# Kernel optimization log

Measured on AMD Instinct MI355X. Metric: run time of the kernel, lower is better.

The kernel has to match this reference:

```python
import jax, jax.numpy as jnp
import numpy as np

B, T, I, H, K = 32, 1024, 512, 512, 2


def _causal_conv1d(x_bit, w_hik, b_h):
    # x_bit: [B, I, T]; left-pad K-1 zeros (ConstantPad1d((K-1, 0)))
    xp = jnp.pad(x_bit, ((0, 0), (0, 0), (K - 1, 0)))
    y = jax.lax.conv_general_dilated(
        xp, w_hik, window_strides=(1,), padding='VALID',
        dimension_numbers=('NCH', 'OIH', 'NCH'))  # [B, H, T]
    return y + b_h[None, :, None]


def setup_inputs() -> dict:
    key = jax.random.key(0)
    k1, k2, k3 = jax.random.split(key, 3)
    bound = 1.0 / np.sqrt(I * K)  # torch Conv1d default init scale
    return {
        'inputs': jax.random.normal(k1, (B, T, I), dtype=jnp.float32),
        'init_state': jnp.zeros((B, H), dtype=jnp.float32),
        'Wz': jax.random.uniform(k2, (H, I, K), jnp.float32, -bound, bound),
        'bz': jnp.zeros((H,), dtype=jnp.float32),
        'Wf': jax.random.uniform(k3, (H, I, K), jnp.float32, -bound, bound),
        'bf': jnp.zeros((H,), dtype=jnp.float32),
    }


def reference(inputs, init_state, Wz, bz, Wf, bf):
    # init_state is accepted but unused in the original forward (mode='f').
    x = inputs.transpose(0, 2, 1)                      # [B, I, T]
    raw_f = _causal_conv1d(x, Wf, bf).transpose(0, 2, 1)  # [B, T, H]
    raw_z = _causal_conv1d(x, Wz, bz).transpose(0, 2, 1)  # [B, T, H]

    log_f = jax.nn.log_sigmoid(raw_f)
    log_one_minus_f = jax.nn.log_sigmoid(-raw_f)
    log_z = jax.nn.log_sigmoid(raw_z)

    # recurrent_gates[t] = sum_{s>t} log_f[s]  (suffix sum of log_f over time, excluding t=0 shift)
    rg = log_f[:, 1:, :]                               # [B, T-1, H]
    cs = jnp.cumsum(rg, axis=1)
    rg = rg - cs + cs[:, -1:, :]
    rg = jnp.concatenate([rg, jnp.zeros((inputs.shape[0], 1, rg.shape[2]), dtype=rg.dtype)], axis=1)  # [B, T, H]

    log_hidden = jax.lax.cumlogsumexp(log_z + log_one_minus_f + rg, axis=1)
    hidden = jnp.exp(log_hidden - rg)
    return hidden
```

## Files before the change

### kernel.cpp

```cpp
#include <hip/hip_runtime.h>
#include <hip/hip_bf16.h>
#include <cstddef>
#include <cstdint>

#define B_  32
#define T_  1024
#define I_  512
#define H_  512
#define M_  (B_ * T_)
#define TP_ 1025

typedef __bf16 bf16x8  __attribute__((ext_vector_type(8)));
typedef float  floatx4 __attribute__((ext_vector_type(4)));
typedef unsigned short ushort8v __attribute__((ext_vector_type(8)));
typedef unsigned long long u64;

__device__ __forceinline__ unsigned short f2bf(float f) {
    return __builtin_bit_cast(unsigned short, (__bf16)f);
}
__device__ __forceinline__ float sigm(float x) {
    return __builtin_amdgcn_rcpf(1.f + __expf(-x));
}

#define GLL(src, dst) __builtin_amdgcn_global_load_lds( \
    (const __attribute__((address_space(1))) void*)(src), \
    (__attribute__((address_space(3))) void*)(dst), 16, 0, 0)

#define NB_BUILD 8200
#define NB_PACK  512
#define NB_ZERO  256

__global__ __launch_bounds__(256) void prep(const float* __restrict__ x,
                                            const float* __restrict__ Wf,
                                            const float* __restrict__ Wz,
                                            unsigned short* __restrict__ Ab2,
                                            unsigned short* __restrict__ Wq,
                                            uint4* __restrict__ HpubZ,
                                            uint32_t* __restrict__ tickets) {
    if (blockIdx.x < NB_BUILD) {
        int g = blockIdx.x * 256 + threadIdx.x;
        int idx8 = g << 3;
        int row = idx8 >> 9;
        int col = idx8 & 511;
        int b    = (int)((unsigned)row / TP_);
        int trow = row - b * TP_;
        ushort8v o = {0, 0, 0, 0, 0, 0, 0, 0};
        if (trow > 0) {
            const float* src = &x[((size_t)b * T_ + (trow - 1)) * I_ + col];
            float4 v0 = *(const float4*)src;
            float4 v1 = *(const float4*)(src + 4);
            o[0] = f2bf(v0.x); o[1] = f2bf(v0.y); o[2] = f2bf(v0.z); o[3] = f2bf(v0.w);
            o[4] = f2bf(v1.x); o[5] = f2bf(v1.y); o[6] = f2bf(v1.z); o[7] = f2bf(v1.w);
        }
        *(ushort8v*)&Ab2[(size_t)idx8] = o;
    } else if (blockIdx.x < NB_BUILD + NB_PACK) {
        int cid = (blockIdx.x - NB_BUILD) * 256 + threadIdx.x;
        int lane = cid & 63;
        int c    = (cid >> 6) & 3;
        int wn   = (cid >> 8) & 1;
        int ksub = (cid >> 9) & 31;
        int ni   = (cid >> 14) & 3;
        int gate = (cid >> 16) & 1;
        int n_col = ni * 128 + wn * 64 + c * 16 + (lane & 15);
        const float* G = gate ? Wz : Wf;
        ushort8v o;
        #pragma unroll
        for (int j = 0; j < 8; ++j) {
            int k   = ksub * 32 + (lane >> 4) * 8 + j;
            int tap = k >> 9;
            int i   = k & 511;
            o[j] = f2bf(G[n_col * (I_ * 2) + i * 2 + tap]);
        }
        *(ushort8v*)&Wq[(size_t)cid * 8] = o;
    } else {
        int g = (blockIdx.x - NB_BUILD - NB_PACK) * 256 + threadIdx.x;
        HpubZ[g] = make_uint4(0, 0, 0, 0);
        if (g < 128) tickets[g] = 0;
    }
}

__global__ __launch_bounds__(256, 2) void mfma_gemm_scan(
        const unsigned short* __restrict__ Ab2,
        const unsigned short* __restrict__ Wq,
        const float* __restrict__ biasF,
        const float* __restrict__ biasZ,
        float* __restrict__ out,
        u64* __restrict__ Hpub,
        uint32_t* __restrict__ tickets) {
    __shared__ unsigned short smem[24576];
    __shared__ uint32_t pos_s;

    const int tid = threadIdx.x;
    const int bid = blockIdx.x;
    const int x   = bid & 7;
    const int ni  = (bid >> 3) & 3;
    const int q   = bid >> 5;
    const int b   = ((q & 3) << 3) | x;
    const int chain = ni * 32 + b;
    if (tid == 0) pos_s = atomicAdd(&tickets[chain], 1u);
    __syncthreads();
    const int pos = (int)pos_s;
    const int h0  = ni * 128;
    const int browBase = b * TP_ + pos * 128;

    const int lane = tid & 63;
    const int wave = tid >> 6;
    const int wm   = wave >> 1, wn = wave & 1;
    const int lm   = lane & 15, quad = lane >> 4;

    const int c0 = wave * 128 + lane;
    const int c1 = c0 + 64;
    const int r0 = c0 >> 2, q0 = (c0 & 3) ^ ((r0 >> 2) & 3);
    const int r1 = c1 >> 2, q1 = (c1 & 3) ^ ((r1 >> 2) & 3);

    const unsigned short* pA0 = Ab2 + (size_t)(browBase + r0) * 512 + q0 * 8;
    const unsigned short* pA1 = Ab2 + (size_t)(browBase + r1) * 512 + q1 * 8;

    const unsigned short* pBF = Wq + ni * 131072 + wn * 2048 + lane * 8;

    int offA[4];
    #pragma unroll
    for (int r = 0; r < 4; ++r) {
        int ml = wm * 64 + r * 16 + lm;
        offA[r] = (4 * ml + (quad ^ ((ml >> 2) & 3))) * 8;
    }

    floatx4 accF[4][4] = {};
    floatx4 accZ[4][4] = {};
    bf16x8 bfA[4], bzA[4], bfB[4], bzB[4];

#define ISSUE_A(ksub, sA) do {                                          \
        const int aoff_ = (((ksub) >> 4) * 512) + (((ksub) & 15) * 32); \
        GLL(pA0 + aoff_, (sA) + wave * 1024);                           \
        GLL(pA1 + aoff_, (sA) + wave * 1024 + 512);                     \
    } while (0)

#define LOADB(ksub, BF, BZ) do {                                        \
        const unsigned short* pf_ = pBF + (ksub) * 4096;                \
        _Pragma("unroll")                                               \
        for (int c = 0; c < 4; ++c) {                                   \
            BF[c] = *(const bf16x8*)(pf_ + c * 512);                    \
            BZ[c] = *(const bf16x8*)(pf_ + 524288 + c * 512);           \
        }                                                               \
    } while (0)

#define MFMA32(AF, BF, BZ) do {                                         \
        __builtin_amdgcn_s_setprio(1);                                  \
        _Pragma("unroll")                                               \
        for (int r = 0; r < 4; ++r) {                                   \
            _Pragma("unroll")                                           \
            for (int c = 0; c < 4; ++c) {                               \
                accF[r][c] = __builtin_amdgcn_mfma_f32_16x16x32_bf16(   \
                                AF[r], BF[c], accF[r][c], 0, 0, 0);     \
                accZ[r][c] = __builtin_amdgcn_mfma_f32_16x16x32_bf16(   \
                                AF[r], BZ[c], accZ[r][c], 0, 0, 0);     \
            }                                                           \
        }                                                               \
        __builtin_amdgcn_s_setprio(0);                                  \
    } while (0)

#define RDA(slot, AF) do {                                              \
        _Pragma("unroll")                                               \
        for (int r = 0; r < 4; ++r)                                     \
            AF[r] = *(const bf16x8*)((slot) + offA[r]);                 \
    } while (0)

#define ROT() do { unsigned short* t_ = s0; s0 = s1; s1 = s2; s2 = t_; } while (0)

    unsigned short* s0 = smem;
    unsigned short* s1 = smem + 4096;
    unsigned short* s2 = smem + 8192;

    ISSUE_A(0, s0);
    ISSUE_A(1, s1);
    LOADB(0, bfA, bzA);

    {
        asm volatile("s_waitcnt vmcnt(0)");
        __builtin_amdgcn_s_barrier();
        asm volatile("" ::: "memory");
        bf16x8 af_[4];
        RDA(s0, af_);
        LOADB(1, bfB, bzB);
        ISSUE_A(2, s2);
        __builtin_amdgcn_sched_barrier(0);
        MFMA32(af_, bfA, bzA);
        ROT();
    }
    for (int p = 0; p < 14; ++p) {
        const int k1 = 2 * p + 1;
        {
            asm volatile("s_waitcnt vmcnt(2)");
            __builtin_amdgcn_s_barrier();
            asm volatile("" ::: "memory");
            bf16x8 af_[4];
            RDA(s0, af_);
            LOADB(k1 + 1, bfA, bzA);
            ISSUE_A(k1 + 2, s2);
            __builtin_amdgcn_sched_barrier(0);
            MFMA32(af_, bfB, bzB);
            ROT();
        }
        {
            asm volatile("s_waitcnt vmcnt(2)");
            __builtin_amdgcn_s_barrier();
            asm volatile("" ::: "memory");
            bf16x8 af_[4];
            RDA(s0, af_);
            LOADB(k1 + 2, bfB, bzB);
            ISSUE_A(k1 + 3, s2);
            __builtin_amdgcn_sched_barrier(0);
            MFMA32(af_, bfA, bzA);
            ROT();
        }
    }
    {
        asm volatile("s_waitcnt vmcnt(2)");
        __builtin_amdgcn_s_barrier();
        asm volatile("" ::: "memory");
        bf16x8 af_[4];
        RDA(s0, af_);
        LOADB(30, bfA, bzA);
        ISSUE_A(31, s2);
        __builtin_amdgcn_sched_barrier(0);
        MFMA32(af_, bfB, bzB);
        ROT();
    }
    {
        asm volatile("s_waitcnt vmcnt(2)");
        __builtin_amdgcn_s_barrier();
        asm volatile("" ::: "memory");
        bf16x8 af_[4];
        RDA(s0, af_);
        LOADB(31, bfB, bzB);
        __builtin_amdgcn_sched_barrier(0);
        MFMA32(af_, bfA, bzA);
        ROT();
    }
    {
        asm volatile("s_waitcnt vmcnt(0)");
        __builtin_amdgcn_s_barrier();
        asm volatile("" ::: "memory");
        bf16x8 af_[4];
        RDA(s0, af_);
        __builtin_amdgcn_sched_barrier(0);
        MFMA32(af_, bfB, bzB);
    }
#undef ISSUE_A
#undef LOADB
#undef MFMA32
#undef RDA
#undef ROT
    __syncthreads();

    float bfv[4], bzv[4];
    #pragma unroll
    for (int c = 0; c < 4; ++c) {
        int hc = h0 + wn * 64 + c * 16 + lm;
        bfv[c] = biasF[hc];
        bzv[c] = biasZ[hc];
    }

    float2* seg  = (float2*)smem;
    float*  hinL = (float*)&smem[16384];

    #pragma unroll
    for (int r = 0; r < 4; ++r) {
        const int sid = wm * 16 + r * 4 + quad;
        #pragma unroll
        for (int c = 0; c < 4; ++c) {
            float A = 1.f, C = 0.f;
            #pragma unroll
            for (int v = 0; v < 4; ++v) {
                float f = sigm(accF[r][c][v] + bfv[c]);
                float z = sigm(accZ[r][c][v] + bzv[c]);
                accF[r][c][v] = f;
                accZ[r][c][v] = z;
                A *= f;
                C = fmaf(f, C - z, z);
            }
            seg[sid * 128 + wn * 64 + c * 16 + lm] = make_float2(A, C);
        }
    }
    __syncthreads();

    if (tid < 128) {
        float At = 1.f, Ct = 0.f;
        #pragma unroll 8
        for (int s = 0; s < 32; ++s) {
            float2 sc = seg[s * 128 + tid];
            Ct = fmaf(sc.x, Ct, sc.y);
            At *= sc.x;
        }
        float Hin = 0.f;
        if (pos > 0) {
            u64* p = &Hpub[((size_t)(pos - 1) * 128 + chain) * 128 + tid];
            u64 v;
            while (((v = atomicAdd(p, 0ull)) >> 32) == 0ull)
                __builtin_amdgcn_s_sleep(2);
            Hin = __uint_as_float((uint32_t)v);
        }
        if (pos < 7) {
            float Hout = fmaf(At, Hin, Ct);
            u64 pv = 0x100000000ull | (u64)__float_as_uint(Hout);
            atomicExch(&Hpub[((size_t)pos * 128 + chain) * 128 + tid], pv);
        }
        float run = Hin;
        #pragma unroll 8
        for (int s = 0; s < 32; ++s) {
            hinL[s * 128 + tid] = run;
            float2 sc = seg[s * 128 + tid];
            run = fmaf(sc.x, run, sc.y);
        }
    }
    __syncthreads();

    const int rowBase = b * T_ + pos * 128;
    #pragma unroll
    for (int r = 0; r < 4; ++r) {
        const int sid = wm * 16 + r * 4 + quad;
        #pragma unroll
        for (int c = 0; c < 4; ++c) {
            const int hc = h0 + wn * 64 + c * 16 + lm;
            float hs = hinL[sid * 128 + (hc - h0)];
            #pragma unroll
            for (int v = 0; v < 4; ++v) {
                float f = accF[r][c][v];
                float z = accZ[r][c][v];
                hs = fmaf(f, hs - z, z);
                const size_t row = (size_t)(rowBase + wm * 64 + r * 16 + quad * 4 + v);
                out[row * H_ + hc] = hs;
            }
        }
    }
}

extern "C" void kernel_launch(void* const* d_in, const int* in_sizes, int n_in,
                              void* d_out, int out_size, void* d_ws, size_t ws_size,
                              hipStream_t stream) {
    const float* x  = (const float*)d_in[0];
    const float* Wz = (const float*)d_in[2];
    const float* bz = (const float*)d_in[3];
    const float* Wf = (const float*)d_in[4];
    const float* bf = (const float*)d_in[5];
    float* out = (float*)d_out;

    char* ws = (char*)d_ws;
    unsigned short* Ab2  = (unsigned short*)(ws);
    unsigned short* Wq   = (unsigned short*)(ws + (size_t)34 * 1024 * 1024);
    u64*            Hpub = (u64*)(ws + (size_t)36 * 1024 * 1024);
    uint32_t*       tkt  = (uint32_t*)(ws + (size_t)37 * 1024 * 1024);

    prep<<<NB_BUILD + NB_PACK + NB_ZERO, 256, 0, stream>>>(
        x, Wf, Wz, Ab2, Wq, (uint4*)Hpub, tkt);

    mfma_gemm_scan<<<1024, 256, 0, stream>>>(Ab2, Wq, bf, bz, out, Hpub, tkt);
}
```

Before: 191.8 us.

## Fuse fp32-to-bf16 input conversion and causal shift into GEMM A-tile loads

```diff
diff --git a/kernel.cpp b/kernel.cpp
--- a/kernel.cpp
+++ b/kernel.cpp
@@ -8,7 +8,6 @@
 #define I_  512
 #define H_  512
 #define M_  (B_ * T_)
-#define TP_ 1025
 
 typedef __bf16 bf16x8  __attribute__((ext_vector_type(8)));
 typedef float  floatx4 __attribute__((ext_vector_type(4)));
@@ -22,39 +21,16 @@
     return __builtin_amdgcn_rcpf(1.f + __expf(-x));
 }
 
-#define GLL(src, dst) __builtin_amdgcn_global_load_lds( \
-    (const __attribute__((address_space(1))) void*)(src), \
-    (__attribute__((address_space(3))) void*)(dst), 16, 0, 0)
-
-#define NB_BUILD 8200
 #define NB_PACK  512
 #define NB_ZERO  256
 
-__global__ __launch_bounds__(256) void prep(const float* __restrict__ x,
-                                            const float* __restrict__ Wf,
+__global__ __launch_bounds__(256) void prep(const float* __restrict__ Wf,
                                             const float* __restrict__ Wz,
-                                            unsigned short* __restrict__ Ab2,
                                             unsigned short* __restrict__ Wq,
                                             uint4* __restrict__ HpubZ,
                                             uint32_t* __restrict__ tickets) {
-    if (blockIdx.x < NB_BUILD) {
-        int g = blockIdx.x * 256 + threadIdx.x;
-        int idx8 = g << 3;
-        int row = idx8 >> 9;
-        int col = idx8 & 511;
-        int b    = (int)((unsigned)row / TP_);
-        int trow = row - b * TP_;
-        ushort8v o = {0, 0, 0, 0, 0, 0, 0, 0};
-        if (trow > 0) {
-            const float* src = &x[((size_t)b * T_ + (trow - 1)) * I_ + col];
-            float4 v0 = *(const float4*)src;
-            float4 v1 = *(const float4*)(src + 4);
-            o[0] = f2bf(v0.x); o[1] = f2bf(v0.y); o[2] = f2bf(v0.z); o[3] = f2bf(v0.w);
-            o[4] = f2bf(v1.x); o[5] = f2bf(v1.y); o[6] = f2bf(v1.z); o[7] = f2bf(v1.w);
-        }
-        *(ushort8v*)&Ab2[(size_t)idx8] = o;
-    } else if (blockIdx.x < NB_BUILD + NB_PACK) {
-        int cid = (blockIdx.x - NB_BUILD) * 256 + threadIdx.x;
+    if (blockIdx.x < NB_PACK) {
+        int cid = blockIdx.x * 256 + threadIdx.x;
         int lane = cid & 63;
         int c    = (cid >> 6) & 3;
         int wn   = (cid >> 8) & 1;
@@ -73,14 +49,14 @@
         }
         *(ushort8v*)&Wq[(size_t)cid * 8] = o;
     } else {
-        int g = (blockIdx.x - NB_BUILD - NB_PACK) * 256 + threadIdx.x;
+        int g = (blockIdx.x - NB_PACK) * 256 + threadIdx.x;
         HpubZ[g] = make_uint4(0, 0, 0, 0);
         if (g < 128) tickets[g] = 0;
     }
 }
 
 __global__ __launch_bounds__(256, 2) void mfma_gemm_scan(
-        const unsigned short* __restrict__ Ab2,
+        const float* __restrict__ x,
         const unsigned short* __restrict__ Wq,
         const float* __restrict__ biasF,
         const float* __restrict__ biasZ,
@@ -92,16 +68,16 @@
 
     const int tid = threadIdx.x;
     const int bid = blockIdx.x;
-    const int x   = bid & 7;
+    const int xcd = bid & 7;
     const int ni  = (bid >> 3) & 3;
     const int q   = bid >> 5;
-    const int b   = ((q & 3) << 3) | x;
+    const int b   = ((q & 3) << 3) | xcd;
     const int chain = ni * 32 + b;
     if (tid == 0) pos_s = atomicAdd(&tickets[chain], 1u);
     __syncthreads();
     const int pos = (int)pos_s;
     const int h0  = ni * 128;
-    const int browBase = b * TP_ + pos * 128;
+    const int trow0 = pos * 128;
 
     const int lane = tid & 63;
     const int wave = tid >> 6;
@@ -113,8 +89,13 @@
     const int r0 = c0 >> 2, q0 = (c0 & 3) ^ ((r0 >> 2) & 3);
     const int r1 = c1 >> 2, q1 = (c1 & 3) ^ ((r1 >> 2) & 3);
 
-    const unsigned short* pA0 = Ab2 + (size_t)(browBase + r0) * 512 + q0 * 8;
-    const unsigned short* pA1 = Ab2 + (size_t)(browBase + r1) * 512 + q1 * 8;
+    const float* zp = (const float*)(Hpub + (size_t)7 * 128 * 128);
+    const float* pt0_r0 = (pos == 0 && r0 == 0)
+        ? (zp + q0 * 8)
+        : (x + (size_t)(b * T_ + trow0 + r0 - 1) * 512 + q0 * 8);
+    const float* pt1_r0 = x + (size_t)(b * T_ + trow0 + r0) * 512 + q0 * 8;
+    const float* pt0_r1 = x + (size_t)(b * T_ + trow0 + r1 - 1) * 512 + q1 * 8;
+    const float* pt1_r1 = x + (size_t)(b * T_ + trow0 + r1) * 512 + q1 * 8;
 
     const unsigned short* pBF = Wq + ni * 131072 + wn * 2048 + lane * 8;
 
@@ -128,11 +109,29 @@
     floatx4 accF[4][4] = {};
     floatx4 accZ[4][4] = {};
     bf16x8 bfA[4], bzA[4], bfB[4], bzB[4];
-
-#define ISSUE_A(ksub, sA) do {                                          \
-        const int aoff_ = (((ksub) >> 4) * 512) + (((ksub) & 15) * 32); \
-        GLL(pA0 + aoff_, (sA) + wave * 1024);                           \
-        GLL(pA1 + aoff_, (sA) + wave * 1024 + 512);                     \
+    float4 av0, av1, av2, av3;
+
+#define LOADA(ksub) do {                                                \
+        const float* b0_ = ((ksub) & 16) ? pt1_r0 : pt0_r0;             \
+        const float* b1_ = ((ksub) & 16) ? pt1_r1 : pt0_r1;             \
+        const int io_ = ((ksub) & 15) * 32;                             \
+        av0 = *(const float4*)(b0_ + io_);                              \
+        av1 = *(const float4*)(b0_ + io_ + 4);                          \
+        av2 = *(const float4*)(b1_ + io_);                              \
+        av3 = *(const float4*)(b1_ + io_ + 4);                          \
+    } while (0)
+
+#define CVTW(slot) do {                                                 \
+        bf16x8 w0_, w1_;                                                \
+        _Pragma("unroll")                                               \
+        for (int j = 0; j < 4; ++j) {                                   \
+            w0_[j]     = (__bf16)av0[j];                                \
+            w0_[4 + j] = (__bf16)av1[j];                                \
+            w1_[j]     = (__bf16)av2[j];                                \
+            w1_[4 + j] = (__bf16)av3[j];                                \
+        }                                                               \
+        *(bf16x8*)((slot) + c0 * 8) = w0_;                              \
+        *(bf16x8*)((slot) + c1 * 8) = w1_;                              \
     } while (0)
 
 #define LOADB(ksub, BF, BZ) do {                                        \
@@ -165,92 +164,86 @@
             AF[r] = *(const bf16x8*)((slot) + offA[r]);                 \
     } while (0)
 
-#define ROT() do { unsigned short* t_ = s0; s0 = s1; s1 = s2; s2 = t_; } while (0)
-
-    unsigned short* s0 = smem;
-    unsigned short* s1 = smem + 4096;
-    unsigned short* s2 = smem + 8192;
-
-    ISSUE_A(0, s0);
-    ISSUE_A(1, s1);
+#define WAITBAR() do {                                                  \
+        asm volatile("s_waitcnt vmcnt(0) lgkmcnt(0)");                  \
+        __builtin_amdgcn_s_barrier();                                   \
+        asm volatile("" ::: "memory");                                  \
+    } while (0)
+
+    unsigned short* sl0 = smem;
+    unsigned short* sl1 = smem + 4096;
+
+    LOADA(0);
+    asm volatile("s_waitcnt vmcnt(0)");
+    CVTW(sl0);
+    LOADA(1);
     LOADB(0, bfA, bzA);
 
+    for (int p = 0; p < 14; ++p) {
+        const int k = 2 * p;
+        {
+            WAITBAR();
+            LOADB(k + 1, bfB, bzB);
+            CVTW(sl1);
+            LOADA(k + 2);
+            __builtin_amdgcn_sched_barrier(0);
+            bf16x8 af_[4];
+            RDA(sl0, af_);
+            MFMA32(af_, bfA, bzA);
+        }
+        {
+            WAITBAR();
+            LOADB(k + 2, bfA, bzA);
+            CVTW(sl0);
+            LOADA(k + 3);
+            __builtin_amdgcn_sched_barrier(0);
+            bf16x8 af_[4];
+            RDA(sl1, af_);
+            MFMA32(af_, bfB, bzB);
+        }
+    }
     {
-        asm volatile("s_waitcnt vmcnt(0)");
-        __builtin_amdgcn_s_barrier();
-        asm volatile("" ::: "memory");
+        WAITBAR();
+        LOADB(29, bfB, bzB);
+        CVTW(sl1);
+        LOADA(30);
+        __builtin_amdgcn_sched_barrier(0);
         bf16x8 af_[4];
-        RDA(s0, af_);
-        LOADB(1, bfB, bzB);
-        ISSUE_A(2, s2);
+        RDA(sl0, af_);
+        MFMA32(af_, bfA, bzA);
+    }
+    {
+        WAITBAR();
+        LOADB(30, bfA, bzA);
+        CVTW(sl0);
+        LOADA(31);
         __builtin_amdgcn_sched_barrier(0);
+        bf16x8 af_[4];
+        RDA(sl1, af_);
+        MFMA32(af_, bfB, bzB);
+    }
+    {
+        WAITBAR();
+        LOADB(31, bfB, bzB);
+        CVTW(sl1);
+        __builtin_amdgcn_sched_barrier(0);
+        bf16x8 af_[4];
+        RDA(sl0, af_);
         MFMA32(af_, bfA, bzA);
-        ROT();
-    }
-    for (int p = 0; p < 14; ++p) {
-        const int k1 = 2 * p + 1;
-        {
-            asm volatile("s_waitcnt vmcnt(2)");
-            __builtin_amdgcn_s_barrier();
-            asm volatile("" ::: "memory");
-            bf16x8 af_[4];
-            RDA(s0, af_);
-            LOADB(k1 + 1, bfA, bzA);
-            ISSUE_A(k1 + 2, s2);
-            __builtin_amdgcn_sched_barrier(0);
-            MFMA32(af_, bfB, bzB);
-            ROT();
-        }
-        {
-            asm volatile("s_waitcnt vmcnt(2)");
-            __builtin_amdgcn_s_barrier();
-            asm volatile("" ::: "memory");
-            bf16x8 af_[4];
-            RDA(s0, af_);
-            LOADB(k1 + 2, bfB, bzB);
-            ISSUE_A(k1 + 3, s2);
-            __builtin_amdgcn_sched_barrier(0);
-            MFMA32(af_, bfA, bzA);
-            ROT();
-        }
     }
     {
-        asm volatile("s_waitcnt vmcnt(2)");
-        __builtin_amdgcn_s_barrier();
-        asm volatile("" ::: "memory");
+        WAITBAR();
+        __builtin_amdgcn_sched_barrier(0);
         bf16x8 af_[4];
-        RDA(s0, af_);
-        LOADB(30, bfA, bzA);
-        ISSUE_A(31, s2);
-        __builtin_amdgcn_sched_barrier(0);
+        RDA(sl1, af_);
         MFMA32(af_, bfB, bzB);
-        ROT();
-    }
-    {
-        asm volatile("s_waitcnt vmcnt(2)");
-        __builtin_amdgcn_s_barrier();
-        asm volatile("" ::: "memory");
-        bf16x8 af_[4];
-        RDA(s0, af_);
-        LOADB(31, bfB, bzB);
-        __builtin_amdgcn_sched_barrier(0);
-        MFMA32(af_, bfA, bzA);
-        ROT();
-    }
-    {
-        asm volatile("s_waitcnt vmcnt(0)");
-        __builtin_amdgcn_s_barrier();
-        asm volatile("" ::: "memory");
-        bf16x8 af_[4];
-        RDA(s0, af_);
-        __builtin_amdgcn_sched_barrier(0);
-        MFMA32(af_, bfB, bzB);
-    }
-#undef ISSUE_A
+    }
+#undef LOADA
+#undef CVTW
 #undef LOADB
 #undef MFMA32
 #undef RDA
-#undef ROT
+#undef WAITBAR
     __syncthreads();
 
     float bfv[4], bzv[4];
@@ -346,13 +339,11 @@
     float* out = (float*)d_out;
 
     char* ws = (char*)d_ws;
-    unsigned short* Ab2  = (unsigned short*)(ws);
-    unsigned short* Wq   = (unsigned short*)(ws + (size_t)34 * 1024 * 1024);
-    u64*            Hpub = (u64*)(ws + (size_t)36 * 1024 * 1024);
-    uint32_t*       tkt  = (uint32_t*)(ws + (size_t)37 * 1024 * 1024);
-
-    prep<<<NB_BUILD + NB_PACK + NB_ZERO, 256, 0, stream>>>(
-        x, Wf, Wz, Ab2, Wq, (uint4*)Hpub, tkt);
-
-    mfma_gemm_scan<<<1024, 256, 0, stream>>>(Ab2, Wq, bf, bz, out, Hpub, tkt);
-}
+    unsigned short* Wq   = (unsigned short*)(ws);
+    u64*            Hpub = (u64*)(ws + (size_t)2 * 1024 * 1024);
+    uint32_t*       tkt  = (uint32_t*)(ws + (size_t)3 * 1024 * 1024);
+
+    prep<<<NB_PACK + NB_ZERO, 256, 0, stream>>>(Wf, Wz, Wq, (uint4*)Hpub, tkt);
+
+    mfma_gemm_scan<<<1024, 256, 0, stream>>>(x, Wq, bf, bz, out, Hpub, tkt);
+}
```

Result: slower. 199.5 us (+4.0%).
